# Performance work log

Hardware: AMD Instinct MI355X
Metric: run time of the kernel (lower is better)

## Reference

```python
import jax, jax.numpy as jnp
import numpy as np

VOC_SIZE = 50000
WORD_DIM = 64
CPR_DIM = 64
NUM_RELS = 7
BATCH = 1024
N_LEAVES = 64  # complete binary tree, depth 6
BOUND = 0.05


def setup_inputs() -> dict:
    key = jax.random.key(0)
    ks = jax.random.split(key, 16)
    u = lambda k, shape: jax.random.uniform(k, shape, jnp.float32, -BOUND, BOUND)
    return {
        "left_leaves": jax.random.randint(ks[0], (BATCH, N_LEAVES), 0, VOC_SIZE),
        "right_leaves": jax.random.randint(ks[1], (BATCH, N_LEAVES), 0, VOC_SIZE),
        "voc_w": u(ks[2], (WORD_DIM, VOC_SIZE)),
        "voc_b": u(ks[3], (WORD_DIM,)),
        "cps_w": u(ks[4], (WORD_DIM, 2 * WORD_DIM)),
        "cps_b": u(ks[5], (WORD_DIM,)),
        "cpst_w": u(ks[6], (WORD_DIM, WORD_DIM * WORD_DIM)),
        "cpst_b": u(ks[7], (WORD_DIM,)),
        "cpr_w": u(ks[8], (CPR_DIM, 2 * WORD_DIM)),
        "cpr_b": u(ks[9], (CPR_DIM,)),
        "cprt_w": u(ks[10], (CPR_DIM, WORD_DIM * WORD_DIM)),
        "cprt_b": u(ks[11], (CPR_DIM,)),
        "sm_w": u(ks[12], (NUM_RELS, CPR_DIM)),
        "sm_b": u(ks[13], (NUM_RELS,)),
    }


def _compose(x, cps_w, cps_b, cpst_w, cpst_b):
    # x: [B, N, d] leaf embeddings of a complete binary tree; reduce level by level.
    B, N, d = x.shape
    while N > 1:
        L = x[:, 0::2, :]  # [B, N/2, d]
        R = x[:, 1::2, :]
        cps = jnp.einsum("bnf,ef->bne", jnp.concatenate([L, R], axis=-1), cps_w) + cps_b
        # NOTE: source computes ger(left, left) for interior nodes (left with itself)
        kron = (L[:, :, :, None] * L[:, :, None, :]).reshape(B, N // 2, d * d)
        cps_t = jnp.einsum("bnk,ek->bne", kron, cpst_w) + cpst_b
        x = jnp.tanh(cps + cps_t)
        N //= 2
    return x[:, 0, :]  # [B, d]


def reference(left_leaves, right_leaves, voc_w, voc_b, cps_w, cps_b, cpst_w, cpst_b,
              cpr_w, cpr_b, cprt_w, cprt_b, sm_w, sm_b):
    # onehot @ Linear == embedding gather of columns of voc_w, plus bias
    left_emb = voc_w.T[left_leaves] + voc_b    # [B, N, d]
    right_emb = voc_w.T[right_leaves] + voc_b
    l = _compose(left_emb, cps_w, cps_b, cpst_w, cpst_b)   # [B, d]
    r = _compose(right_emb, cps_w, cps_b, cpst_w, cpst_b)  # [B, d]
    cpr = jnp.concatenate([l, r], axis=-1) @ cpr_w.T + cpr_b
    kron = (l[:, :, None] * r[:, None, :]).reshape(l.shape[0], -1)  # [B, d*d]
    cpr_t = kron @ cprt_w.T + cprt_b
    act = jax.nn.leaky_relu(cpr + cpr_t, negative_slope=0.01)
    logits = act @ sm_w.T + sm_b
    return jax.nn.softmax(logits, axis=-1)  # [B, num_rels]
```

## Files before the change

### kernel.cpp

```cpp
#include <hip/hip_runtime.h>
#include <hip/hip_bf16.h>
#include <cstdint>
#include <cstddef>

typedef _Float16 f16x8 __attribute__((ext_vector_type(8)));
typedef float    f32x4 __attribute__((ext_vector_type(4)));

#define VOC    50000
#define W2T    2432
#define NSTG_T 19
#define W2F    4224
#define NSTG_F 33
#define STG    8192
#define XSTR   72
#define TPW    8
#define IPW    16

__device__ __attribute__((aligned(256))) unsigned short g_vocT[(size_t)VOC * 64];
__device__ __attribute__((aligned(256))) unsigned short g_roots[2048 * 64];
__device__ __attribute__((aligned(256))) unsigned short g_cpstU[(size_t)NSTG_T * STG];
__device__ __attribute__((aligned(256))) unsigned short g_cprtU[(size_t)NSTG_F * STG];
__device__ float g_smw[7 * 64];
__device__ float g_smb[7];
__device__ float g_biasC[64];
__device__ float g_biasF[64];

#define KE(BI0,BJ0,R0,BI1,BJ1,R1) \
    ((BI0) | ((BJ0) << 3) | ((R0) << 6) | ((BI1) << 7) | ((BJ1) << 10) | ((R1) << 13))
__device__ __constant__ int g_ktab[18] = {
    KE(0,0,1, 0,1,1), KE(0,2,0, 0,3,0), KE(0,4,0, 0,5,0), KE(0,6,0, 0,7,0),
    KE(1,1,1, 1,2,1), KE(1,3,0, 1,4,0), KE(1,5,0, 1,6,0), KE(1,7,0, 2,2,1),
    KE(2,3,1, 2,4,0), KE(2,5,0, 2,6,0), KE(2,7,0, 3,3,1), KE(3,4,1, 3,5,0),
    KE(3,6,0, 3,7,0), KE(4,4,1, 4,5,1), KE(4,6,0, 4,7,0), KE(5,5,1, 5,6,1),
    KE(5,7,0, 6,6,1), KE(6,7,1, 7,7,1)
};

__device__ __forceinline__ float b2f(unsigned short u) {
    unsigned int x = ((unsigned int)u) << 16;
    return __builtin_bit_cast(float, x);
}
__device__ __forceinline__ unsigned short f2b(float f) {
    return __builtin_bit_cast(unsigned short, (__bf16)f);
}
__device__ __forceinline__ unsigned short f2h(float f) {
    return __builtin_bit_cast(unsigned short, (_Float16)f);
}
__device__ __forceinline__ float scrub(float v) {
    return fminf(fmaxf(v, -64.f), 64.f);
}
__device__ __forceinline__ float ldf(const void* p, size_t i, int isb) {
    return isb ? b2f(((const unsigned short*)p)[i]) : ((const float*)p)[i];
}
__device__ __forceinline__ int detect_isb(const void* voc_b) {
    const unsigned int* p = (const unsigned int*)voc_b;
    int ok = 1;
    for (int k = 0; k < 32; k++) {
        float v = b2f((unsigned short)(p[k] & 0xFFFFu));
        if (!(fabsf(v) <= 0.0502f)) ok = 0;
    }
    return ok;
}

__global__ __launch_bounds__(256) void k_prep(
    const void* voc_w, const void* voc_b,
    const void* cps_w, const void* cps_b, const void* cpst_w, const void* cpst_b,
    const void* cpr_w, const void* cpr_b, const void* cprt_w, const void* cprt_b,
    const void* sm_w, const void* sm_b)
{
    __shared__ float tile[64][65];
    __shared__ float vb[64];
    const int isb = detect_isb(voc_b);
    if (blockIdx.x < 512) {
        int gid = blockIdx.x * 256 + threadIdx.x;
        int stride = 512 * 256;
        for (int d = gid; d < 64 * W2T; d += stride) {
            int s    = d / STG;
            int rem  = d - s * STG;
            int kbl  = rem >> 11;
            int rem2 = rem & 2047;
            int nt   = rem2 >> 9;
            int rem3 = rem2 & 511;
            int q    = rem3 >> 7;
            int rem4 = rem3 & 127;
            int sub  = rem4 >> 3;
            int z    = rem4 & 7;
            int n    = nt * 16 + sub;
            int k    = s * 128 + kbl * 32 + q * 8 + z;
            float w;
            if (k < 2304) {
                int b   = k >> 6;
                int p2l = (k >> 5) & 1;
                int bi = 0, remb = b;
                while (remb >= 8 - bi) { remb -= 8 - bi; bi++; }
                int bj = bi + remb;
                int i = bi * 8 + z;
                int j = bj * 8 + 2 * q + p2l;
                w = ldf(cpst_w, (size_t)n * 4096 + i * 64 + j, isb);
                if (bi != bj)
                    w += ldf(cpst_w, (size_t)n * 4096 + j * 64 + i, isb);
            } else {
                w = ldf(cps_w, (size_t)n * 128 + (k - 2304), isb);
            }
            g_cpstU[d] = f2h(w);
        }
        for (int d = gid; d < 64 * W2F; d += stride) {
            int s    = d / STG;
            int rem  = d - s * STG;
            int kbl  = rem >> 11;
            int rem2 = rem & 2047;
            int nt   = rem2 >> 9;
            int rem3 = rem2 & 511;
            int q    = rem3 >> 7;
            int rem4 = rem3 & 127;
            int sub  = rem4 >> 3;
            int z    = rem4 & 7;
            int n    = nt * 16 + sub;
            int k    = s * 128 + kbl * 32 + q * 8 + z;
            float v2 = (k < 4096) ? ldf(cprt_w, (size_t)n * 4096 + k, isb)
                                  : ldf(cpr_w,  (size_t)n * 128 + (k - 4096), isb);
            g_cprtU[d] = f2h(v2);
        }
        for (int i = gid; i < 448; i += stride) g_smw[i] = ldf(sm_w, i, isb);
        if (gid < 64) {
            g_biasC[gid] = ldf(cps_b, gid, isb) + ldf(cpst_b, gid, isb);
            g_biasF[gid] = ldf(cpr_b, gid, isb) + ldf(cprt_b, gid, isb);
        }
        if (gid < 7) g_smb[gid] = ldf(sm_b, gid, isb);
    } else {
        int t = threadIdx.x;
        if (t < 64) vb[t] = ldf(voc_b, t, isb);
        int v0 = (blockIdx.x - 512) * 64;
        int vl = t & 63, dr = t >> 6;
        #pragma unroll
        for (int i = 0; i < 16; i++) {
            int d = dr * 16 + i;
            int v = v0 + vl;
            tile[vl][d] = (v < VOC) ? ldf(voc_w, (size_t)d * VOC + v, isb) : 0.f;
        }
        __syncthreads();
        int dl = t & 63, vr0 = t >> 6;
        #pragma unroll
        for (int i = 0; i < 16; i++) {
            int vr = vr0 * 16 + i;
            int v = v0 + vr;
            if (v < VOC) g_vocT[(size_t)v * 64 + dl] = f2h(tile[vr][dl] + vb[dl]);
        }
    }
}

#define EPILOGUE(CO)                                                          \
    {                                                                         \
        _Pragma("unroll")                                                     \
        for (int nt = 0; nt < 4; nt++) {                                      \
            int e = nt * 16 + sub;                                            \
            _Pragma("unroll")                                                 \
            for (int rr = 0; rr < 4; rr++) {                                  \
                int m = chv[CO] * 16 + q * 4 + rr;                            \
                if (m < nodes) {                                              \
                    int t2 = m >> lg, n2 = m & (cnew - 1);                    \
                    Xs[(t2 * 64 + n2) * XSTR + e] =                           \
                        f2h(tanhf(scrub(acc[CO][nt][rr] + biasC[e])));        \
                }                                                             \
            }                                                                 \
        }                                                                     \
    }

#define EXSEND(CS)                                                            \
    { _Pragma("unroll")                                                       \
      for (int nt = 0; nt < 4; nt++)                                          \
          *(f32x4*)(exchS + wave * 1024 + nt * 256 + lane * 4) = acc[CS][nt]; }

#define EXRECV(CO)                                                            \
    { _Pragma("unroll")                                                       \
      for (int nt = 0; nt < 4; nt++) {                                        \
          f32x4 v_ = *(const f32x4*)(exchS + (wave ^ 1) * 1024 + nt * 256 + lane * 4); \
          _Pragma("unroll")                                                   \
          for (int z = 0; z < 4; z++) acc[CO][nt][z] += v_[z];                \
      } }

#define BLD8(BF, SBASE)                                                       \
    { const unsigned short* gs_ = (SBASE) + half * 4096 + lane * 8;           \
      _Pragma("unroll")                                                       \
      for (int j = 0; j < 8; j++)                                             \
          BF[j] = *(const f16x8*)(gs_ + (j >> 2) * 2048 + (j & 3) * 512); }

#define KMM(CI, AV, B0, B1, B2, B3)                                           \
    { f16x8 a_ = (AV);                                                        \
      acc[CI][0] = __builtin_amdgcn_mfma_f32_16x16x32_f16(a_, B0, acc[CI][0], 0, 0, 0); \
      acc[CI][1] = __builtin_amdgcn_mfma_f32_16x16x32_f16(a_, B1, acc[CI][1], 0, 0, 0); \
      acc[CI][2] = __builtin_amdgcn_mfma_f32_16x16x32_f16(a_, B2, acc[CI][2], 0, 0, 0); \
      acc[CI][3] = __builtin_amdgcn_mfma_f32_16x16x32_f16(a_, B3, acc[CI][3], 0, 0, 0); }

#define KBLOCKR(BF, BI, BJ, RLD)                                              \
    if (act[0]) {                                                             \
        if (RLD) {                                                            \
            lA0 = *(const f16x8*)(Xs + slotL[0] + (BI) * 8);                  \
            if (act[1]) lA1 = *(const f16x8*)(Xs + slotL[1] + (BI) * 8);      \
            if (act[2]) lA2 = *(const f16x8*)(Xs + slotL[2] + (BI) * 8);      \
            if (act[3]) lA3 = *(const f16x8*)(Xs + slotL[3] + (BI) * 8);      \
        }                                                                     \
        _Float16 sc0[4], sc1[4];                                              \
        _Pragma("unroll")                                                     \
        for (int c = 0; c < 4; c++)                                           \
            if (act[c]) {                                                     \
                unsigned pr_ = *(const unsigned*)(Xs + slotL[c] + (BJ) * 8 + 2 * q); \
                sc0[c] = __builtin_bit_cast(_Float16, (unsigned short)(pr_ & 0xFFFFu)); \
                sc1[c] = __builtin_bit_cast(_Float16, (unsigned short)(pr_ >> 16));     \
            }                                                                 \
        _Pragma("unroll")                                                     \
        for (int p2 = 0; p2 < 2; p2++) {                                      \
            KMM(0, lA0 * (p2 ? sc1[0] : sc0[0]),                              \
                BF[p2 * 4 + 0], BF[p2 * 4 + 1], BF[p2 * 4 + 2], BF[p2 * 4 + 3]) \
            if (act[1]) KMM(1, lA1 * (p2 ? sc1[1] : sc0[1]),                  \
                BF[p2 * 4 + 0], BF[p2 * 4 + 1], BF[p2 * 4 + 2], BF[p2 * 4 + 3]) \
            if (act[2]) KMM(2, lA2 * (p2 ? sc1[2] : sc0[2]),                  \
                BF[p2 * 4 + 0], BF[p2 * 4 + 1], BF[p2 * 4 + 2], BF[p2 * 4 + 3]) \
            if (act[3]) KMM(3, lA3 * (p2 ? sc1[3] : sc0[3]),                  \
                BF[p2 * 4 + 0], BF[p2 * 4 + 1], BF[p2 * 4 + 2], BF[p2 * 4 + 3]) \
        }                                                                     \
    }

#define KRUNR(S, BF)                                                          \
    {                                                                         \
        int e_   = g_ktab[S];                                                 \
        int ent_ = half ? (e_ >> 7) : e_;                                     \
        int bi_  = ent_ & 7;                                                  \
        int bj_  = (ent_ >> 3) & 7;                                           \
        int rld_ = (ent_ >> 6) & 1;                                           \
        KBLOCKR((BF), bi_, bj_, rld_)                                         \
    }

#define DBLD2(BF, SBASE)                                                      \
    { const unsigned short* gs_ = (SBASE) + half * 4096 + lane * 8;           \
      BF[0] = *(const f16x8*)(gs_ + (ntb + 0) * 512);                         \
      BF[1] = *(const f16x8*)(gs_ + (ntb + 1) * 512);                         \
      BF[2] = *(const f16x8*)(gs_ + 2048 + (ntb + 0) * 512);                  \
      BF[3] = *(const f16x8*)(gs_ + 2048 + (ntb + 1) * 512); }

#define DBLD1(BF, SBASE)                                                      \
    { const unsigned short* gs_ = (SBASE) + half * 4096 + ntb * 512 + lane * 8; \
      BF[0] = *(const f16x8*)(gs_);                                           \
      BF[1] = *(const f16x8*)(gs_ + 2048); }

#define DKRUN2(S, BF)                                                         \
    {                                                                         \
        int e_   = g_ktab[S];                                                 \
        int ent_ = half ? (e_ >> 7) : e_;                                     \
        int bi_  = ent_ & 7;                                                  \
        int bj_  = (ent_ >> 3) & 7;                                           \
        if ((ent_ >> 6) & 1) lAD = *(const f16x8*)(Xs + slotD + bi_ * 8);     \
        unsigned pr_ = *(const unsigned*)(Xs + slotD + bj_ * 8 + 2 * q);      \
        _Float16 s0_ = __builtin_bit_cast(_Float16, (unsigned short)(pr_ & 0xFFFFu)); \
        _Float16 s1_ = __builtin_bit_cast(_Float16, (unsigned short)(pr_ >> 16));     \
        f16x8 a0_ = lAD * s0_;                                                \
        accD0 = __builtin_amdgcn_mfma_f32_16x16x32_f16(a0_, BF[0], accD0, 0, 0, 0); \
        accD1 = __builtin_amdgcn_mfma_f32_16x16x32_f16(a0_, BF[1], accD1, 0, 0, 0); \
        f16x8 a1_ = lAD * s1_;                                                \
        accD0 = __builtin_amdgcn_mfma_f32_16x16x32_f16(a1_, BF[2], accD0, 0, 0, 0); \
        accD1 = __builtin_amdgcn_mfma_f32_16x16x32_f16(a1_, BF[3], accD1, 0, 0, 0); \
    }

#define DKRUN1(S, BF)                                                         \
    {                                                                         \
        int e_   = g_ktab[S];                                                 \
        int ent_ = half ? (e_ >> 7) : e_;                                     \
        int bi_  = ent_ & 7;                                                  \
        int bj_  = (ent_ >> 3) & 7;                                           \
        if ((ent_ >> 6) & 1) lAD = *(const f16x8*)(Xs + slotD + bi_ * 8);     \
        unsigned pr_ = *(const unsigned*)(Xs + slotD + bj_ * 8 + 2 * q);      \
        _Float16 s0_ = __builtin_bit_cast(_Float16, (unsigned short)(pr_ & 0xFFFFu)); \
        _Float16 s1_ = __builtin_bit_cast(_Float16, (unsigned short)(pr_ >> 16));     \
        accD0 = __builtin_amdgcn_mfma_f32_16x16x32_f16(lAD * s0_, BF[0], accD0, 0, 0, 0); \
        accD0 = __builtin_amdgcn_mfma_f32_16x16x32_f16(lAD * s1_, BF[1], accD0, 0, 0, 0); \
    }

__global__ __launch_bounds__(512, 2)
void k_tree(const int* __restrict__ lleaf, const int* __restrict__ rleaf)
{
    __shared__ __attribute__((aligned(16))) unsigned short Xs[512 * XSTR];
    __shared__ __attribute__((aligned(16))) float exchS[8192];
    __shared__ float biasC[64];
    const int tid = threadIdx.x;
    const int wg  = blockIdx.x;

    if (tid < 64) biasC[tid] = g_biasC[tid];

    {
        int t = tid >> 6, i = tid & 63;
        int gidx = wg * TPW + t;
        int b = (gidx < 1024) ? gidx : gidx - 1024;
        const int* lv2 = (gidx < 1024) ? lleaf : rleaf;
        int idx = lv2[b * 64 + i];
        idx = (idx < 0) ? 0 : ((idx >= VOC) ? VOC - 1 : idx);
        const uint4* src = (const uint4*)(g_vocT + (size_t)idx * 64);
        uint4* dst = (uint4*)(Xs + tid * XSTR);
        #pragma unroll
        for (int z = 0; z < 8; z++) dst[z] = src[z];
    }

    __syncthreads();

    const int lane = tid & 63, wave = tid >> 6;
    const int q = lane >> 4, sub = lane & 15;
    const int p = wave >> 1, half = wave & 1;

    #pragma unroll 1
    for (int lv = 0; lv < 6; lv++) {
        const int lg = 5 - lv;
        const int cnew = 1 << lg;
        const int nodes = TPW << lg;
        const int nchunks = (nodes + 15) >> 4;

        if (nchunks >= 4) {
            int act[4], chv[4], slotL[4];
            #pragma unroll
            for (int c = 0; c < 4; c++) {
                int ch = p + 4 * c;
                act[c] = (ch < nchunks);
                chv[c] = ch;
                int m = ch * 16 + sub;
                if (!act[c] || m >= nodes) m = 0;
                int t = m >> lg, n = m & (cnew - 1);
                slotL[c] = (t * 64 + 2 * n) * XSTR;
            }

            f16x8 lA0 = {}, lA1 = {}, lA2 = {}, lA3 = {};
            f32x4 acc[4][4];
            #pragma unroll
            for (int c = 0; c < 4; c++)
                #pragma unroll
                for (int nt = 0; nt < 4; nt++)
                    #pragma unroll
                    for (int z = 0; z < 4; z++) acc[c][nt][z] = 0.f;

            f16x8 bfA[8], bfB[8];
            if (act[0]) BLD8(bfA, g_cpstU)
            #pragma unroll 1
            for (int t = 0; t < 9; t++) {
                if (act[0]) BLD8(bfB, g_cpstU + (size_t)(2 * t + 1) * STG)
                KRUNR(2 * t, bfA)
                if (act[0]) BLD8(bfA, g_cpstU + (size_t)(2 * t + 2) * STG)
                KRUNR(2 * t + 1, bfB)
            }
            if (act[0]) {
                #pragma unroll
                for (int p2 = 0; p2 < 2; p2++) {
                    #pragma unroll
                    for (int c = 0; c < 4; c++) {
                        if (!act[c]) continue;
                        f16x8 A = *(const f16x8*)(Xs + slotL[c] + half * XSTR + p2 * 32 + q * 8);
                        acc[c][0] = __builtin_amdgcn_mfma_f32_16x16x32_f16(A, bfA[p2 * 4 + 0], acc[c][0], 0, 0, 0);
                        acc[c][1] = __builtin_amdgcn_mfma_f32_16x16x32_f16(A, bfA[p2 * 4 + 1], acc[c][1], 0, 0, 0);
                        acc[c][2] = __builtin_amdgcn_mfma_f32_16x16x32_f16(A, bfA[p2 * 4 + 2], acc[c][2], 0, 0, 0);
                        acc[c][3] = __builtin_amdgcn_mfma_f32_16x16x32_f16(A, bfA[p2 * 4 + 3], acc[c][3], 0, 0, 0);
                    }
                }
            }

            if (half == 0) { if (act[1]) EXSEND(1) } else { if (act[0]) EXSEND(0) }
            __syncthreads();
            if (half == 0) {
                if (act[0]) { EXRECV(0) EPILOGUE(0) }
            } else {
                if (act[1]) { EXRECV(1) EPILOGUE(1) }
            }
            __syncthreads();
            if (half == 0) { if (act[3]) EXSEND(3) } else { if (act[2]) EXSEND(2) }
            __syncthreads();
            if (half == 0) {
                if (act[2]) { EXRECV(2) EPILOGUE(2) }
            } else {
                if (act[3]) { EXRECV(3) EPILOGUE(3) }
            }
            __syncthreads();
        } else if (nchunks == 2) {
            const int chD = p >> 1;
            const int ntb = (p & 1) * 2;
            int mD = chD * 16 + sub;
            int tD = mD >> lg, nD = mD & (cnew - 1);
            const int slotD = (tD * 64 + 2 * nD) * XSTR;
            f16x8 lAD = {};
            f32x4 accD0 = {0.f,0.f,0.f,0.f}, accD1 = {0.f,0.f,0.f,0.f};

            f16x8 dA[4], dB[4];
            DBLD2(dA, g_cpstU)
            #pragma unroll 1
            for (int t = 0; t < 9; t++) {
                DBLD2(dB, g_cpstU + (size_t)(2 * t + 1) * STG)
                DKRUN2(2 * t, dA)
                DBLD2(dA, g_cpstU + (size_t)(2 * t + 2) * STG)
                DKRUN2(2 * t + 1, dB)
            }
            {
                #pragma unroll
                for (int p2 = 0; p2 < 2; p2++) {
                    f16x8 A = *(const f16x8*)(Xs + slotD + half * XSTR + p2 * 32 + q * 8);
                    accD0 = __builtin_amdgcn_mfma_f32_16x16x32_f16(A, dA[p2 * 2 + 0], accD0, 0, 0, 0);
                    accD1 = __builtin_amdgcn_mfma_f32_16x16x32_f16(A, dA[p2 * 2 + 1], accD1, 0, 0, 0);
                }
            }
            if (half == 1) {
                *(f32x4*)(exchS + p * 1024 + lane * 4) = accD0;
                *(f32x4*)(exchS + p * 1024 + 256 + lane * 4) = accD1;
            }
            __syncthreads();
            if (half == 0) {
                {   f32x4 v0 = *(const f32x4*)(exchS + p * 1024 + lane * 4);
                    f32x4 v1 = *(const f32x4*)(exchS + p * 1024 + 256 + lane * 4);
                    #pragma unroll
                    for (int z = 0; z < 4; z++) { accD0[z] += v0[z]; accD1[z] += v1[z]; }
                }
                #pragma unroll
                for (int j = 0; j < 2; j++) {
                    int e = (ntb + j) * 16 + sub;
                    #pragma unroll
                    for (int rr = 0; rr < 4; rr++) {
                        int m = chD * 16 + q * 4 + rr;
                        int t2 = m >> lg, n2 = m & (cnew - 1);
                        float av = j ? accD1[rr] : accD0[rr];
                        Xs[(t2 * 64 + n2) * XSTR + e] = f2h(tanhf(scrub(av + biasC[e])));
                    }
                }
            }
            __syncthreads();
        } else {
            const int ntb = p;
            int mD = sub;
            if (mD >= nodes) mD = 0;
            int tD = mD >> lg, nD = mD & (cnew - 1);
            const int slotD = (tD * 64 + 2 * nD) * XSTR;
            f16x8 lAD = {};
            f32x4 accD0 = {0.f,0.f,0.f,0.f};

            f16x8 dA[2], dB[2];
            DBLD1(dA, g_cpstU)
            #pragma unroll 1
            for (int t = 0; t < 9; t++) {
                DBLD1(dB, g_cpstU + (size_t)(2 * t + 1) * STG)
                DKRUN1(2 * t, dA)
                DBLD1(dA, g_cpstU + (size_t)(2 * t + 2) * STG)
                DKRUN1(2 * t + 1, dB)
            }
            {
                #pragma unroll
                for (int p2 = 0; p2 < 2; p2++) {
                    f16x8 A = *(const f16x8*)(Xs + slotD + half * XSTR + p2 * 32 + q * 8);
                    accD0 = __builtin_amdgcn_mfma_f32_16x16x32_f16(A, dA[p2], accD0, 0, 0, 0);
                }
            }
            if (half == 1)
                *(f32x4*)(exchS + p * 1024 + lane * 4) = accD0;
            __syncthreads();
            if (half == 0) {
                {   f32x4 v0 = *(const f32x4*)(exchS + p * 1024 + lane * 4);
                    #pragma unroll
                    for (int z = 0; z < 4; z++) accD0[z] += v0[z];
                }
                int e = ntb * 16 + sub;
                if (lv < 5) {
                    #pragma unroll
                    for (int rr = 0; rr < 4; rr++) {
                        int m = q * 4 + rr;
                        int t2 = m >> lg, n2 = m & (cnew - 1);
                        Xs[(t2 * 64 + n2) * XSTR + e] = f2h(tanhf(scrub(accD0[rr] + biasC[e])));
                    }
                } else {
                    #pragma unroll
                    for (int rr = 0; rr < 4; rr++) {
                        int m = q * 4 + rr;
                        if (m < TPW)
                            g_roots[((size_t)wg * TPW + m) * 64 + e] =
                                f2h(tanhf(scrub(accD0[rr] + biasC[e])));
                    }
                }
            }
            __syncthreads();
        }
    }
}

#define BLD4(BF, S)                                                           \
    { const unsigned short* gs_ = g_cprtU + (size_t)(S) * STG + w * 512 + lane * 8; \
      _Pragma("unroll")                                                       \
      for (int j = 0; j < 4; j++)                                             \
          BF[j] = *(const f16x8*)(gs_ + j * 2048); }

#define FKRONR(S, BF)                                                         \
    { _Pragma("unroll")                                                       \
      for (int ii = 0; ii < 2; ii++) {                                        \
          int i_ = 2 * (S) + ii;                                              \
          _Float16 li_ = __builtin_bit_cast(_Float16, Lv[rowLo + i_]);        \
          _Pragma("unroll")                                                   \
          for (int p2 = 0; p2 < 2; p2++) {                                    \
              f16x8 afr_ = Ra[p2] * li_;                                      \
              acc = __builtin_amdgcn_mfma_f32_16x16x32_f16(afr_, BF[2 * ii + p2], acc, 0, 0, 0); \
          }                                                                   \
      } }

__global__ __launch_bounds__(256, 2) void k_final(const void* __restrict__ voc_b,
                                                  void* __restrict__ out)
{
    __shared__ __attribute__((aligned(16))) unsigned short Lv[IPW * XSTR], Rv[IPW * XSTR];
    __shared__ float actS[IPW][65];
    __shared__ float smw[7][64];
    __shared__ float smbS[7];
    __shared__ float biasF[64];
    const int tid = threadIdx.x, wg = blockIdx.x;
    const int isb = detect_isb(voc_b);

    if (tid < 64) biasF[tid] = g_biasF[tid];
    if (tid < 7)  smbS[tid] = g_smb[tid];
    for (int z = tid; z < 448; z += 256) smw[z >> 6][z & 63] = g_smw[z];

    {
        int side = tid >> 7, idx = tid & 127;
        int item = idx >> 3, piece = idx & 7;
        const uint4* s4 = (const uint4*)(g_roots +
            ((size_t)(side * 1024) + (size_t)wg * IPW + item) * 64 + piece * 8);
        uint4* d4 = (uint4*)((side ? Rv : Lv) + item * XSTR + piece * 8);
        *d4 = *s4;
    }

    const int lane = tid & 63, w = tid >> 6;
    const int q = lane >> 4, sub = lane & 15;
    const int rowLo = sub * XSTR;

    f16x8 bA[4], bB[4];
    BLD4(bA, 0)

    __syncthreads();

    f16x8 Ra[2];
    Ra[0] = *(const f16x8*)(Rv + rowLo + q * 8);
    Ra[1] = *(const f16x8*)(Rv + rowLo + 32 + q * 8);

    f32x4 acc;
    #pragma unroll
    for (int z = 0; z < 4; z++) acc[z] = 0.f;

    #pragma unroll 1
    for (int t = 0; t < 16; t++) {
        BLD4(bB, 2 * t + 1)
        FKRONR(2 * t, bA)
        BLD4(bA, 2 * t + 2)
        FKRONR(2 * t + 1, bB)
    }

    {
        f16x8 A4[4];
        A4[0] = *(const f16x8*)(Lv + rowLo + q * 8);
        A4[1] = *(const f16x8*)(Lv + rowLo + 32 + q * 8);
        A4[2] = *(const f16x8*)(Rv + rowLo + q * 8);
        A4[3] = *(const f16x8*)(Rv + rowLo + 32 + q * 8);
        #pragma unroll
        for (int kbl = 0; kbl < 4; kbl++)
            acc = __builtin_amdgcn_mfma_f32_16x16x32_f16(A4[kbl], bA[kbl], acc, 0, 0, 0);
    }

    {
        int e = w * 16 + sub;
        #pragma unroll
        for (int rr = 0; rr < 4; rr++) {
            int item = q * 4 + rr;
            float v = scrub(acc[rr] + biasF[e]);
            v = (v > 0.f) ? v : 0.01f * v;
            actS[item][e] = v;
        }
    }
    __syncthreads();

    if (tid < IPW) {
        float lg[7];
        #pragma unroll
        for (int j = 0; j < 7; j++) lg[j] = smbS[j];
        for (int e = 0; e < 64; e++) {
            float a = actS[tid][e];
            #pragma unroll
            for (int j = 0; j < 7; j++) lg[j] += smw[j][e] * a;
        }
        float mx = lg[0];
        #pragma unroll
        for (int j = 1; j < 7; j++) mx = fmaxf(mx, lg[j]);
        float s = 0.f, pr[7];
        #pragma unroll
        for (int j = 0; j < 7; j++) { pr[j] = expf(lg[j] - mx); s += pr[j]; }
        float inv = 1.f / s;
        size_t b = (size_t)wg * IPW + tid;
        if (isb) {
            unsigned short* o = (unsigned short*)out;
            #pragma unroll
            for (int j = 0; j < 7; j++) o[b * 7 + j] = f2b(pr[j] * inv);
        } else {
            float* o = (float*)out;
            #pragma unroll
            for (int j = 0; j < 7; j++) o[b * 7 + j] = pr[j] * inv;
        }
    }
}

extern "C" void kernel_launch(void* const* d_in, const int* in_sizes, int n_in,
                              void* d_out, int out_size, void* d_ws, size_t ws_size,
                              hipStream_t stream) {
    const int* lleaf = (const int*)d_in[0];
    const int* rleaf = (const int*)d_in[1];
    const void* voc_w  = d_in[2];
    const void* voc_b  = d_in[3];
    const void* cps_w  = d_in[4];
    const void* cps_b  = d_in[5];
    const void* cpst_w = d_in[6];
    const void* cpst_b = d_in[7];
    const void* cpr_w  = d_in[8];
    const void* cpr_b  = d_in[9];
    const void* cprt_w = d_in[10];
    const void* cprt_b = d_in[11];
    const void* sm_w   = d_in[12];
    const void* sm_b   = d_in[13];

    k_prep<<<512 + (VOC + 63) / 64, 256, 0, stream>>>(
        voc_w, voc_b, cps_w, cps_b, cpst_w, cpst_b,
        cpr_w, cpr_b, cprt_w, cprt_b, sm_w, sm_b);
    k_tree<<<2048 / TPW, 512, 0, stream>>>(lleaf, rleaf);
    k_final<<<64, 256, 0, stream>>>(voc_b, (unsigned short*)d_out);
}
```

Measured before the change: 165.6 us.

## Double tree-kernel block to 1024 threads and repartition level work across waves

The tree-reduction kernel now launches 1024 threads per workgroup instead of 512. Each wave handles at most two row chunks instead of four. The small levels are split further by output tile and by K-slices across the extra waves, with a partial-sum exchange through shared memory. The intent is more waves in flight to hide MFMA and load latency and fewer serial chunks per wave. The cost is extra barriers and exchange traffic, plus register pressure under the new launch bounds.

```diff
diff --git a/kernel.cpp b/kernel.cpp
--- a/kernel.cpp
+++ b/kernel.cpp
@@ -50,6 +50,12 @@
 }
 __device__ __forceinline__ float ldf(const void* p, size_t i, int isb) {
     return isb ? b2f(((const unsigned short*)p)[i]) : ((const float*)p)[i];
+}
+__device__ __forceinline__ _Float16 lo16(unsigned u) {
+    return __builtin_bit_cast(_Float16, (unsigned short)(u & 0xFFFFu));
+}
+__device__ __forceinline__ _Float16 hi16(unsigned u) {
+    return __builtin_bit_cast(_Float16, (unsigned short)(u >> 16));
 }
 __device__ __forceinline__ int detect_isb(const void* voc_b) {
     const unsigned int* p = (const unsigned int*)voc_b;
@@ -148,87 +154,66 @@
     }
 }
 
-#define EPILOGUE(CO)                                                          \
-    {                                                                         \
-        _Pragma("unroll")                                                     \
-        for (int nt = 0; nt < 4; nt++) {                                      \
-            int e = nt * 16 + sub;                                            \
-            _Pragma("unroll")                                                 \
-            for (int rr = 0; rr < 4; rr++) {                                  \
-                int m = chv[CO] * 16 + q * 4 + rr;                            \
-                if (m < nodes) {                                              \
-                    int t2 = m >> lg, n2 = m & (cnew - 1);                    \
-                    Xs[(t2 * 64 + n2) * XSTR + e] =                           \
-                        f2h(tanhf(scrub(acc[CO][nt][rr] + biasC[e])));        \
-                }                                                             \
-            }                                                                 \
-        }                                                                     \
-    }
-
-#define EXSEND(CS)                                                            \
-    { _Pragma("unroll")                                                       \
-      for (int nt = 0; nt < 4; nt++)                                          \
-          *(f32x4*)(exchS + wave * 1024 + nt * 256 + lane * 4) = acc[CS][nt]; }
-
-#define EXRECV(CO)                                                            \
-    { _Pragma("unroll")                                                       \
-      for (int nt = 0; nt < 4; nt++) {                                        \
-          f32x4 v_ = *(const f32x4*)(exchS + (wave ^ 1) * 1024 + nt * 256 + lane * 4); \
-          _Pragma("unroll")                                                   \
-          for (int z = 0; z < 4; z++) acc[CO][nt][z] += v_[z];                \
-      } }
-
 #define BLD8(BF, SBASE)                                                       \
     { const unsigned short* gs_ = (SBASE) + half * 4096 + lane * 8;           \
       _Pragma("unroll")                                                       \
       for (int j = 0; j < 8; j++)                                             \
           BF[j] = *(const f16x8*)(gs_ + (j >> 2) * 2048 + (j & 3) * 512); }
 
-#define KMM(CI, AV, B0, B1, B2, B3)                                           \
+#define KMM(CI, AV, BF, P2)                                                   \
     { f16x8 a_ = (AV);                                                        \
-      acc[CI][0] = __builtin_amdgcn_mfma_f32_16x16x32_f16(a_, B0, acc[CI][0], 0, 0, 0); \
-      acc[CI][1] = __builtin_amdgcn_mfma_f32_16x16x32_f16(a_, B1, acc[CI][1], 0, 0, 0); \
-      acc[CI][2] = __builtin_amdgcn_mfma_f32_16x16x32_f16(a_, B2, acc[CI][2], 0, 0, 0); \
-      acc[CI][3] = __builtin_amdgcn_mfma_f32_16x16x32_f16(a_, B3, acc[CI][3], 0, 0, 0); }
-
-#define KBLOCKR(BF, BI, BJ, RLD)                                              \
-    if (act[0]) {                                                             \
+      acc[CI][0] = __builtin_amdgcn_mfma_f32_16x16x32_f16(a_, BF[(P2)*4+0], acc[CI][0], 0, 0, 0); \
+      acc[CI][1] = __builtin_amdgcn_mfma_f32_16x16x32_f16(a_, BF[(P2)*4+1], acc[CI][1], 0, 0, 0); \
+      acc[CI][2] = __builtin_amdgcn_mfma_f32_16x16x32_f16(a_, BF[(P2)*4+2], acc[CI][2], 0, 0, 0); \
+      acc[CI][3] = __builtin_amdgcn_mfma_f32_16x16x32_f16(a_, BF[(P2)*4+3], acc[CI][3], 0, 0, 0); }
+
+#define KBLOCKA(BF, BI, BJ, RLD)                                              \
+    {                                                                         \
         if (RLD) {                                                            \
-            lA0 = *(const f16x8*)(Xs + slotL[0] + (BI) * 8);                  \
-            if (act[1]) lA1 = *(const f16x8*)(Xs + slotL[1] + (BI) * 8);      \
-            if (act[2]) lA2 = *(const f16x8*)(Xs + slotL[2] + (BI) * 8);      \
-            if (act[3]) lA3 = *(const f16x8*)(Xs + slotL[3] + (BI) * 8);      \
+            lA0 = *(const f16x8*)(Xs + slotL0 + (BI) * 8);                    \
+            if (act1) lA1 = *(const f16x8*)(Xs + slotL1 + (BI) * 8);          \
         }                                                                     \
-        _Float16 sc0[4], sc1[4];                                              \
-        _Pragma("unroll")                                                     \
-        for (int c = 0; c < 4; c++)                                           \
-            if (act[c]) {                                                     \
-                unsigned pr_ = *(const unsigned*)(Xs + slotL[c] + (BJ) * 8 + 2 * q); \
-                sc0[c] = __builtin_bit_cast(_Float16, (unsigned short)(pr_ & 0xFFFFu)); \
-                sc1[c] = __builtin_bit_cast(_Float16, (unsigned short)(pr_ >> 16));     \
-            }                                                                 \
-        _Pragma("unroll")                                                     \
-        for (int p2 = 0; p2 < 2; p2++) {                                      \
-            KMM(0, lA0 * (p2 ? sc1[0] : sc0[0]),                              \
-                BF[p2 * 4 + 0], BF[p2 * 4 + 1], BF[p2 * 4 + 2], BF[p2 * 4 + 3]) \
-            if (act[1]) KMM(1, lA1 * (p2 ? sc1[1] : sc0[1]),                  \
-                BF[p2 * 4 + 0], BF[p2 * 4 + 1], BF[p2 * 4 + 2], BF[p2 * 4 + 3]) \
-            if (act[2]) KMM(2, lA2 * (p2 ? sc1[2] : sc0[2]),                  \
-                BF[p2 * 4 + 0], BF[p2 * 4 + 1], BF[p2 * 4 + 2], BF[p2 * 4 + 3]) \
-            if (act[3]) KMM(3, lA3 * (p2 ? sc1[3] : sc0[3]),                  \
-                BF[p2 * 4 + 0], BF[p2 * 4 + 1], BF[p2 * 4 + 2], BF[p2 * 4 + 3]) \
-        }                                                                     \
-    }
-
-#define KRUNR(S, BF)                                                          \
+        unsigned pr0_ = *(const unsigned*)(Xs + slotL0 + (BJ) * 8 + 2 * q);   \
+        unsigned pr1_ = act1 ? *(const unsigned*)(Xs + slotL1 + (BJ) * 8 + 2 * q) : 0; \
+        KMM(0, lA0 * lo16(pr0_), BF, 0)                                       \
+        if (act1) KMM(1, lA1 * lo16(pr1_), BF, 0)                             \
+        KMM(0, lA0 * hi16(pr0_), BF, 1)                                       \
+        if (act1) KMM(1, lA1 * hi16(pr1_), BF, 1)                             \
+    }
+
+#define KRUNA(S, BF)                                                          \
     {                                                                         \
         int e_   = g_ktab[S];                                                 \
         int ent_ = half ? (e_ >> 7) : e_;                                     \
         int bi_  = ent_ & 7;                                                  \
         int bj_  = (ent_ >> 3) & 7;                                           \
         int rld_ = (ent_ >> 6) & 1;                                           \
-        KBLOCKR((BF), bi_, bj_, rld_)                                         \
-    }
+        KBLOCKA((BF), bi_, bj_, rld_)                                         \
+    }
+
+#define EXSENDA(CS)                                                           \
+    { _Pragma("unroll")                                                       \
+      for (int nt = 0; nt < 4; nt++)                                          \
+          *(f32x4*)(exchS + p * 1024 + nt * 256 + lane * 4) = acc[CS][nt]; }
+#define EXRECVA(CO)                                                           \
+    { _Pragma("unroll")                                                       \
+      for (int nt = 0; nt < 4; nt++) {                                        \
+          f32x4 v_ = *(const f32x4*)(exchS + p * 1024 + nt * 256 + lane * 4); \
+          _Pragma("unroll")                                                   \
+          for (int z = 0; z < 4; z++) acc[CO][nt][z] += v_[z];                \
+      } }
+#define EPIA(CHV, CO)                                                         \
+    { _Pragma("unroll")                                                       \
+      for (int nt = 0; nt < 4; nt++) {                                        \
+          int e = nt * 16 + sub;                                              \
+          _Pragma("unroll")                                                   \
+          for (int rr = 0; rr < 4; rr++) {                                    \
+              int m = (CHV) * 16 + q * 4 + rr;                                \
+              int t2 = m >> lg, n2 = m & (cnew - 1);                          \
+              Xs[(t2 * 64 + n2) * XSTR + e] =                                 \
+                  f2h(tanhf(scrub(acc[CO][nt][rr] + biasC[e])));              \
+          }                                                                   \
+      } }
 
 #define DBLD2(BF, SBASE)                                                      \
     { const unsigned short* gs_ = (SBASE) + half * 4096 + lane * 8;           \
@@ -250,12 +235,10 @@
         int bj_  = (ent_ >> 3) & 7;                                           \
         if ((ent_ >> 6) & 1) lAD = *(const f16x8*)(Xs + slotD + bi_ * 8);     \
         unsigned pr_ = *(const unsigned*)(Xs + slotD + bj_ * 8 + 2 * q);      \
-        _Float16 s0_ = __builtin_bit_cast(_Float16, (unsigned short)(pr_ & 0xFFFFu)); \
-        _Float16 s1_ = __builtin_bit_cast(_Float16, (unsigned short)(pr_ >> 16));     \
-        f16x8 a0_ = lAD * s0_;                                                \
+        f16x8 a0_ = lAD * lo16(pr_);                                          \
         accD0 = __builtin_amdgcn_mfma_f32_16x16x32_f16(a0_, BF[0], accD0, 0, 0, 0); \
         accD1 = __builtin_amdgcn_mfma_f32_16x16x32_f16(a0_, BF[1], accD1, 0, 0, 0); \
-        f16x8 a1_ = lAD * s1_;                                                \
+        f16x8 a1_ = lAD * hi16(pr_);                                          \
         accD0 = __builtin_amdgcn_mfma_f32_16x16x32_f16(a1_, BF[2], accD0, 0, 0, 0); \
         accD1 = __builtin_amdgcn_mfma_f32_16x16x32_f16(a1_, BF[3], accD1, 0, 0, 0); \
     }
@@ -268,13 +251,11 @@
         int bj_  = (ent_ >> 3) & 7;                                           \
         if ((ent_ >> 6) & 1) lAD = *(const f16x8*)(Xs + slotD + bi_ * 8);     \
         unsigned pr_ = *(const unsigned*)(Xs + slotD + bj_ * 8 + 2 * q);      \
-        _Float16 s0_ = __builtin_bit_cast(_Float16, (unsigned short)(pr_ & 0xFFFFu)); \
-        _Float16 s1_ = __builtin_bit_cast(_Float16, (unsigned short)(pr_ >> 16));     \
-        accD0 = __builtin_amdgcn_mfma_f32_16x16x32_f16(lAD * s0_, BF[0], accD0, 0, 0, 0); \
-        accD0 = __builtin_amdgcn_mfma_f32_16x16x32_f16(lAD * s1_, BF[1], accD0, 0, 0, 0); \
-    }
-
-__global__ __launch_bounds__(512, 2)
+        accD0 = __builtin_amdgcn_mfma_f32_16x16x32_f16(lAD * lo16(pr_), BF[0], accD0, 0, 0, 0); \
+        accD0 = __builtin_amdgcn_mfma_f32_16x16x32_f16(lAD * hi16(pr_), BF[1], accD0, 0, 0, 0); \
+    }
+
+__global__ __launch_bounds__(1024, 4)
 void k_tree(const int* __restrict__ lleaf, const int* __restrict__ rleaf)
 {
     __shared__ __attribute__((aligned(16))) unsigned short Xs[512 * XSTR];
@@ -286,16 +267,17 @@
     if (tid < 64) biasC[tid] = g_biasC[tid];
 
     {
-        int t = tid >> 6, i = tid & 63;
+        int r = tid >> 1, ph = tid & 1;
+        int t = r >> 6, i = r & 63;
         int gidx = wg * TPW + t;
         int b = (gidx < 1024) ? gidx : gidx - 1024;
         const int* lv2 = (gidx < 1024) ? lleaf : rleaf;
         int idx = lv2[b * 64 + i];
         idx = (idx < 0) ? 0 : ((idx >= VOC) ? VOC - 1 : idx);
-        const uint4* src = (const uint4*)(g_vocT + (size_t)idx * 64);
-        uint4* dst = (uint4*)(Xs + tid * XSTR);
-        #pragma unroll
-        for (int z = 0; z < 8; z++) dst[z] = src[z];
+        const uint4* src = (const uint4*)(g_vocT + (size_t)idx * 64) + ph * 4;
+        uint4* dst = (uint4*)(Xs + r * XSTR) + ph * 4;
+        #pragma unroll
+        for (int z = 0; z < 4; z++) dst[z] = src[z];
     }
 
     __syncthreads();
@@ -311,74 +293,59 @@
         const int nodes = TPW << lg;
         const int nchunks = (nodes + 15) >> 4;
 
-        if (nchunks >= 4) {
-            int act[4], chv[4], slotL[4];
+        if (nchunks >= 8) {
+            const int act1 = (nchunks == 16);
+            int slotL0, slotL1;
+            {
+                int m0 = p * 16 + sub;
+                slotL0 = ((m0 >> lg) * 64 + 2 * (m0 & (cnew - 1))) * XSTR;
+                int m1 = act1 ? ((p + 8) * 16 + sub) : 0;
+                slotL1 = ((m1 >> lg) * 64 + 2 * (m1 & (cnew - 1))) * XSTR;
+            }
+            f16x8 lA0 = {}, lA1 = {};
+            f32x4 acc[2][4];
             #pragma unroll
-            for (int c = 0; c < 4; c++) {
-                int ch = p + 4 * c;
-                act[c] = (ch < nchunks);
-                chv[c] = ch;
-                int m = ch * 16 + sub;
-                if (!act[c] || m >= nodes) m = 0;
-                int t = m >> lg, n = m & (cnew - 1);
-                slotL[c] = (t * 64 + 2 * n) * XSTR;
-            }
-
-            f16x8 lA0 = {}, lA1 = {}, lA2 = {}, lA3 = {};
-            f32x4 acc[4][4];
-            #pragma unroll
-            for (int c = 0; c < 4; c++)
+            for (int c = 0; c < 2; c++)
                 #pragma unroll
                 for (int nt = 0; nt < 4; nt++)
                     #pragma unroll
                     for (int z = 0; z < 4; z++) acc[c][nt][z] = 0.f;
 
             f16x8 bfA[8], bfB[8];
-            if (act[0]) BLD8(bfA, g_cpstU)
+            BLD8(bfA, g_cpstU)
             #pragma unroll 1
             for (int t = 0; t < 9; t++) {
-                if (act[0]) BLD8(bfB, g_cpstU + (size_t)(2 * t + 1) * STG)
-                KRUNR(2 * t, bfA)
-                if (act[0]) BLD8(bfA, g_cpstU + (size_t)(2 * t + 2) * STG)
-                KRUNR(2 * t + 1, bfB)
-            }
-            if (act[0]) {
+                BLD8(bfB, g_cpstU + (size_t)(2 * t + 1) * STG)
+                KRUNA(2 * t, bfA)
+                BLD8(bfA, g_cpstU + (size_t)(2 * t + 2) * STG)
+                KRUNA(2 * t + 1, bfB)
+            }
+            {
                 #pragma unroll
                 for (int p2 = 0; p2 < 2; p2++) {
-                    #pragma unroll
-                    for (int c = 0; c < 4; c++) {
-                        if (!act[c]) continue;
-                        f16x8 A = *(const f16x8*)(Xs + slotL[c] + half * XSTR + p2 * 32 + q * 8);
-                        acc[c][0] = __builtin_amdgcn_mfma_f32_16x16x32_f16(A, bfA[p2 * 4 + 0], acc[c][0], 0, 0, 0);
-                        acc[c][1] = __builtin_amdgcn_mfma_f32_16x16x32_f16(A, bfA[p2 * 4 + 1], acc[c][1], 0, 0, 0);
-                        acc[c][2] = __builtin_amdgcn_mfma_f32_16x16x32_f16(A, bfA[p2 * 4 + 2], acc[c][2], 0, 0, 0);
-                        acc[c][3] = __builtin_amdgcn_mfma_f32_16x16x32_f16(A, bfA[p2 * 4 + 3], acc[c][3], 0, 0, 0);
+                    f16x8 A0 = *(const f16x8*)(Xs + slotL0 + half * XSTR + p2 * 32 + q * 8);
+                    KMM(0, A0, bfA, p2)
+                    if (act1) {
+                        f16x8 A1 = *(const f16x8*)(Xs + slotL1 + half * XSTR + p2 * 32 + q * 8);
+                        KMM(1, A1, bfA, p2)
                     }
                 }
             }
-
-            if (half == 0) { if (act[1]) EXSEND(1) } else { if (act[0]) EXSEND(0) }
-            __syncthreads();
-            if (half == 0) {
-                if (act[0]) { EXRECV(0) EPILOGUE(0) }
-            } else {
-                if (act[1]) { EXRECV(1) EPILOGUE(1) }
-            }
-            __syncthreads();
-            if (half == 0) { if (act[3]) EXSEND(3) } else { if (act[2]) EXSEND(2) }
-            __syncthreads();
-            if (half == 0) {
-                if (act[2]) { EXRECV(2) EPILOGUE(2) }
-            } else {
-                if (act[3]) { EXRECV(3) EPILOGUE(3) }
-            }
-            __syncthreads();
-        } else if (nchunks == 2) {
+            if (half == 1) EXSENDA(0)
+            __syncthreads();
+            if (half == 0) { EXRECVA(0) EPIA(p, 0) }
+            __syncthreads();
+            if (act1) {
+                if (half == 0) EXSENDA(1)
+                __syncthreads();
+                if (half == 1) { EXRECVA(1) EPIA(p + 8, 1) }
+                __syncthreads();
+            }
+        } else if (nchunks == 4) {
             const int chD = p >> 1;
             const int ntb = (p & 1) * 2;
             int mD = chD * 16 + sub;
-            int tD = mD >> lg, nD = mD & (cnew - 1);
-            const int slotD = (tD * 64 + 2 * nD) * XSTR;
+            const int slotD = ((mD >> lg) * 64 + 2 * (mD & (cnew - 1))) * XSTR;
             f16x8 lAD = {};
             f32x4 accD0 = {0.f,0.f,0.f,0.f}, accD1 = {0.f,0.f,0.f,0.f};
 
@@ -423,12 +390,11 @@
                 }
             }
             __syncthreads();
-        } else {
-            const int ntb = p;
-            int mD = sub;
-            if (mD >= nodes) mD = 0;
-            int tD = mD >> lg, nD = mD & (cnew - 1);
-            const int slotD = (tD * 64 + 2 * nD) * XSTR;
+        } else if (nchunks == 2) {
+            const int chD = p >> 2;
+            const int ntb = p & 3;
+            int mD = chD * 16 + sub;
+            const int slotD = ((mD >> lg) * 64 + 2 * (mD & (cnew - 1))) * XSTR;
             f16x8 lAD = {};
             f32x4 accD0 = {0.f,0.f,0.f,0.f};
 
@@ -453,6 +419,53 @@
             __syncthreads();
             if (half == 0) {
                 {   f32x4 v0 = *(const f32x4*)(exchS + p * 1024 + lane * 4);
+                    #pragma unroll
+                    for (int z = 0; z < 4; z++) accD0[z] += v0[z];
+                }
+                int e = ntb * 16 + sub;
+                #pragma unroll
+                for (int rr = 0; rr < 4; rr++) {
+                    int m = chD * 16 + q * 4 + rr;
+                    int t2 = m >> lg, n2 = m & (cnew - 1);
+                    Xs[(t2 * 64 + n2) * XSTR + e] = f2h(tanhf(scrub(accD0[rr] + biasC[e])));
+                }
+            }
+            __syncthreads();
+        } else {
+            const int ntb = p & 3;
+            const int kh  = p >> 2;
+            int mD = sub;
+            if (mD >= nodes) mD = 0;
+            const int slotD = ((mD >> lg) * 64 + 2 * (mD & (cnew - 1))) * XSTR;
+            f16x8 lAD = {};
+            f32x4 accD0 = {0.f,0.f,0.f,0.f};
+
+            f16x8 dA[2], dB[2];
+            DBLD1(dA, g_cpstU + (size_t)kh * STG)
+            #pragma unroll 1
+            for (int i = 0; i < 4; i++) {
+                DBLD1(dB, g_cpstU + (size_t)(kh + 4 * i + 2) * STG)
+                DKRUN1(kh + 4 * i, dA)
+                DBLD1(dA, g_cpstU + (size_t)(kh + 4 * i + 4) * STG)
+                DKRUN1(kh + 4 * i + 2, dB)
+            }
+            DKRUN1(kh + 16, dA)
+            {
+                const int kbl = 2 * kh + half;
+                f16x8 A = *(const f16x8*)(Xs + slotD + kh * XSTR + half * 32 + q * 8);
+                f16x8 Bc = *(const f16x8*)(g_cpstU + (size_t)18 * STG + kbl * 2048 + ntb * 512 + lane * 8);
+                accD0 = __builtin_amdgcn_mfma_f32_16x16x32_f16(A, Bc, accD0, 0, 0, 0);
+            }
+            {
+                int key = kh * 2 + half;
+                if (key != 0)
+                    *(f32x4*)(exchS + (ntb * 3 + key - 1) * 256 + lane * 4) = accD0;
+            }
+            __syncthreads();
+            if (kh == 0 && half == 0) {
+                #pragma unroll
+                for (int sx = 0; sx < 3; sx++) {
+                    f32x4 v0 = *(const f32x4*)(exchS + (ntb * 3 + sx) * 256 + lane * 4);
                     #pragma unroll
                     for (int z = 0; z < 4; z++) accD0[z] += v0[z];
                 }
@@ -619,6 +632,6 @@
     k_prep<<<512 + (VOC + 63) / 64, 256, 0, stream>>>(
         voc_w, voc_b, cps_w, cps_b, cpst_w, cpst_b,
         cpr_w, cpr_b, cprt_w, cprt_b, sm_w, sm_b);
-    k_tree<<<2048 / TPW, 512, 0, stream>>>(lleaf, rleaf);
+    k_tree<<<2048 / TPW, 1024, 0, stream>>>(lleaf, rleaf);
     k_final<<<64, 256, 0, stream>>>(voc_b, (unsigned short*)d_out);
 }
```

Measured after the change: 206.9 us. 1.25x slower.
